# Performance work log

Hardware: AMD Instinct MI355X
Metric: run time of the kernel (lower is better)

Reference implementation:

```python
import jax, jax.numpy as jnp
import numpy as np

N = 100000          # nodes
E = 800000          # edges per relation
R = 6               # relations
B = 1000            # graphs
IN_DIM = 14
POS_COL = 5
PE = 8              # pos_emb_dim
H = 128             # hidden_dim
OUT = 128           # out_dim
NPOS = 24
D1 = IN_DIM - 1 + PE  # 21, GAT layer-1 input dim


def setup_inputs() -> dict:
    key = jax.random.key(0)
    ks = jax.random.split(key, 20)
    x_all = jax.random.normal(ks[0], (N, IN_DIM), dtype=jnp.float32)
    pos = jax.random.randint(ks[1], (N,), 0, NPOS)
    x_all = x_all.at[:, POS_COL].set(pos.astype(jnp.float32))
    edges = jax.random.randint(ks[2], (R, 2, E), 0, N, dtype=jnp.int32)
    batch = jnp.sort(jax.random.randint(ks[3], (N,), 0, B, dtype=jnp.int32))
    pos_table = jax.random.normal(ks[4], (NPOS, PE), dtype=jnp.float32) * 0.02
    W1 = jax.random.normal(ks[5], (R, D1, H), dtype=jnp.float32) * 0.1
    as1 = jax.random.normal(ks[6], (R, H), dtype=jnp.float32) * 0.1
    ad1 = jax.random.normal(ks[7], (R, H), dtype=jnp.float32) * 0.1
    b1 = jnp.zeros((R, H), dtype=jnp.float32)
    W2 = jax.random.normal(ks[8], (R, H, H), dtype=jnp.float32) * 0.05
    as2 = jax.random.normal(ks[9], (R, H), dtype=jnp.float32) * 0.1
    ad2 = jax.random.normal(ks[10], (R, H), dtype=jnp.float32) * 0.1
    b2 = jnp.zeros((R, H), dtype=jnp.float32)
    n1w = jnp.ones((H,), dtype=jnp.float32)
    n1b = jnp.zeros((H,), dtype=jnp.float32)
    n2w = jnp.ones((H,), dtype=jnp.float32)
    n2b = jnp.zeros((H,), dtype=jnp.float32)
    query = jax.random.normal(ks[11], (H,), dtype=jnp.float32) * 0.02
    projW = jax.random.normal(ks[12], (H, OUT), dtype=jnp.float32) * 0.05
    projb = jnp.zeros((OUT,), dtype=jnp.float32)
    return dict(x_all=x_all, edges=edges, batch=batch, pos_table=pos_table,
                W1=W1, as1=as1, ad1=ad1, b1=b1, W2=W2, as2=as2, ad2=ad2, b2=b2,
                n1w=n1w, n1b=n1b, n2w=n2w, n2b=n2b, query=query, projW=projW, projb=projb)


def _seg_softmax(logits, seg, num):
    m = jax.lax.stop_gradient(jax.ops.segment_max(logits, seg, num_segments=num))
    e = jnp.exp(logits - m[seg])
    s = jax.ops.segment_sum(e, seg, num_segments=num)
    return e / s[seg]


def _gat_layer(x, W, a_s, a_d, b, edges):
    # sum over R relation-specific GATConv(heads=1, concat=False) outputs
    n = x.shape[0]
    out = jnp.zeros((n, W.shape[-1]), dtype=x.dtype)
    for r in range(R):
        xp = x @ W[r]                       # [N, H] projected features
        src, dst = edges[r, 0], edges[r, 1]
        z = (xp @ a_s[r])[src] + (xp @ a_d[r])[dst]
        z = jnp.where(z > 0, z, 0.2 * z)    # LeakyReLU(0.2)
        alpha = _seg_softmax(z, dst, n)     # per-destination softmax
        agg = jax.ops.segment_sum(alpha[:, None] * xp[src], dst, num_segments=n)
        out = out + agg + b[r]
    return out


def _ln(x, w, b):
    mu = x.mean(-1, keepdims=True)
    v = ((x - mu) ** 2).mean(-1, keepdims=True)
    return (x - mu) / jnp.sqrt(v + 1e-5) * w + b


def reference(x_all, edges, batch, pos_table, W1, as1, ad1, b1,
              W2, as2, ad2, b2, n1w, n1b, n2w, n2b, query, projW, projb):
    cont = jnp.concatenate([x_all[:, :POS_COL], x_all[:, POS_COL + 1:]], axis=1)
    pidx = jnp.clip(x_all[:, POS_COL].astype(jnp.int32), 0, NPOS - 1)
    x = jnp.concatenate([cont, pos_table[pidx]], axis=1)  # [N, D1]
    x = _gat_layer(x, W1, as1, ad1, b1, edges)
    x = _ln(jax.nn.gelu(x, approximate=False), n1w, n1b)
    x = _gat_layer(x, W2, as2, ad2, b2, edges)
    x = _ln(jax.nn.gelu(x, approximate=False), n2w, n2b)
    # AttentionPooling: gather-score-softmax-scatter over batch segments
    scores = x @ query
    w = _seg_softmax(scores, batch, B)
    pool = jax.ops.segment_sum(w[:, None] * x, batch, num_segments=B)  # [B, H]
    return pool @ projW + projb
```

## Files before the change

kernel.cpp:

```cpp
#include <hip/hip_runtime.h>
#include <math.h>

#define NN   100000
#define EE   800000
#define RR   6
#define BB   1000
#define HH   128
#define MM   (RR*NN)
#define NBPR ((NN + 255) >> 8)
#define NBK  (RR * NBPR)
#define CH   4096
#define CAP  4096

static inline int ceil_div(int a, int b){ return (a+b-1)/b; }

typedef __attribute__((ext_vector_type(8))) short bf16x8;
typedef __attribute__((ext_vector_type(4))) short bf16x4;
typedef __attribute__((ext_vector_type(4))) float f32x4;

__device__ __forceinline__ unsigned fenc(float f){
  unsigned u = __float_as_uint(f);
  return (u & 0x80000000u) ? ~u : (u | 0x80000000u);
}
__device__ __forceinline__ float fdec(unsigned u){
  return __uint_as_float((u & 0x80000000u) ? (u & 0x7fffffffu) : ~u);
}
__device__ __forceinline__ unsigned short f2bf(float f){
  unsigned u = __float_as_uint(f);
  return (unsigned short)((u + 0x7fffu + ((u >> 16) & 1u)) >> 16);
}
__device__ __forceinline__ float bf2f(unsigned short h){
  return __uint_as_float(((unsigned)h) << 16);
}
__device__ __forceinline__ float wexp(float z){
  z = (z > 0.f) ? z : 0.2f*z;
  z = fminf(fmaxf(z, -60.f), 60.f);
  return __expf(z);
}

__global__ void k_binscatter(const int* __restrict__ edges, int* __restrict__ bcur,
                             unsigned* __restrict__ ebkt)
{
  __shared__ int hist[NBPR];
  __shared__ int base[NBPR];
  int t = threadIdx.x;
  const int nch = (EE + CH - 1) / CH;
  int r = blockIdx.x / nch, c = blockIdx.x - r*nch;
  for (int i = t; i < NBPR; i += 256) hist[i] = 0;
  __syncthreads();
  const int* sptr = edges + (size_t)r*2*EE;
  const int* dptr = sptr + EE;
  int e0 = c*CH, e1 = min(EE, e0 + CH);
  for (int i = e0 + t; i < e1; i += 256)
    atomicAdd(&hist[dptr[i] >> 8], 1);
  __syncthreads();
  for (int i = t; i < NBPR; i += 256) {
    int h = hist[i];
    int gb = r*NBPR + i;
    base[i] = h ? (gb*CAP + atomicAdd(&bcur[gb], h)) : 0;
    hist[i] = 0;
  }
  __syncthreads();
  for (int i = e0 + t; i < e1; i += 256) {
    int dst = dptr[i];
    int b = dst >> 8;
    int slot = base[b] + atomicAdd(&hist[b], 1);
    ebkt[slot] = ((unsigned)sptr[i] << 8) | (unsigned)(dst & 255);
  }
}

__global__ void k_bscan(const int* __restrict__ bcur, int* __restrict__ boff,
                        int* __restrict__ off)
{
  __shared__ int sh[256];
  int t = threadIdx.x;
  int carry = 0;
  for (int c = 0; c < NBK; c += 256) {
    int idx = c + t;
    int v = (idx < NBK) ? bcur[idx] : 0;
    sh[t] = v;
    __syncthreads();
    for (int o = 1; o < 256; o <<= 1) {
      int add = (t >= o) ? sh[t-o] : 0;
      __syncthreads();
      sh[t] += add;
      __syncthreads();
    }
    int incl = sh[t];
    int tot  = sh[255];
    if (idx < NBK) boff[idx] = carry + incl - v;
    __syncthreads();
    carry += tot;
  }
  if (t == 0) { boff[NBK] = carry; off[MM] = carry; }
}

__global__ void k_bbuild(const unsigned* __restrict__ ebkt, const int* __restrict__ bcur,
                         const int* __restrict__ boff,
                         int* __restrict__ off, int* __restrict__ elist)
{
  __shared__ int cnt[256];
  __shared__ int sc[256];
  __shared__ int cur[256];
  int t = threadIdx.x;
  int bb = blockIdx.x;
  int e0r = bb*CAP, e1r = e0r + bcur[bb];
  int w0 = boff[bb];
  cnt[t] = 0;
  __syncthreads();
  for (int i = e0r + t; i < e1r; i += 256)
    atomicAdd(&cnt[ebkt[i] & 255u], 1);
  __syncthreads();
  sc[t] = cnt[t];
  __syncthreads();
  for (int o = 1; o < 256; o <<= 1) {
    int add = (t >= o) ? sc[t-o] : 0;
    __syncthreads();
    sc[t] += add;
    __syncthreads();
  }
  int excl = sc[t] - cnt[t];
  int r = bb / NBPR, b = bb - r*NBPR;
  int dst = b*256 + t;
  if (dst < NN) off[r*NN + dst] = w0 + excl;
  cur[t] = w0 + excl;
  __syncthreads();
  for (int i = e0r + t; i < e1r; i += 256) {
    unsigned w = ebkt[i];
    int slot = atomicAdd(&cur[w & 255u], 1);
    elist[slot] = (int)(w >> 8);
  }
}

__global__ void k_featprep(const float* __restrict__ x_all, const float* __restrict__ pos_table,
                           short* __restrict__ x0h, short* __restrict__ x0l)
{
  int gid = blockIdx.x*256 + threadIdx.x;
  if (gid >= NN*32) return;
  int nidx = gid >> 5, c = gid & 31;
  float v = 0.f;
  if (c < 13) {
    int scl = (c < 5) ? c : c + 1;
    v = x_all[nidx*14 + scl];
  } else if (c < 21) {
    int pi = (int)x_all[nidx*14 + 5];
    pi = pi < 0 ? 0 : (pi > 23 ? 23 : pi);
    v = pos_table[pi*8 + (c - 13)];
  }
  unsigned short h = f2bf(v);
  unsigned short l = f2bf(v - bf2f(h));
  x0h[gid] = (short)h;
  x0l[gid] = (short)l;
}

template<int KP>
__global__ void k_wprep(const float* __restrict__ W, int K,
                        short* __restrict__ Wh, short* __restrict__ Wl)
{
  int gid = blockIdx.x*256 + threadIdx.x;
  if (gid >= RR*128*KP) return;
  int r = gid / (128*KP);
  int rem = gid - r*(128*KP);
  int nn = rem / KP, k = rem - nn*KP;
  float v = (k < K) ? W[((size_t)r*K + k)*128 + nn] : 0.f;
  unsigned short h = f2bf(v);
  unsigned short l = f2bf(v - bf2f(h));
  Wh[gid] = (short)h;
  Wl[gid] = (short)l;
}

__global__ void k_wprep2(const float* __restrict__ W,
                         short* __restrict__ Wh, short* __restrict__ Wl)
{
  int gid = blockIdx.x*256 + threadIdx.x;
  if (gid >= RR*128*128) return;
  int r = gid / (128*128);
  int i = gid - r*(128*128);
  int kc = i >> 12;
  int lg = (i >> 10) & 3;
  int row = (i >> 3) & 127;
  int e = i & 7;
  int k = kc*32 + 16*(e >> 2) + 4*lg + (e & 3);
  float v = W[((size_t)r*128 + k)*128 + row];
  unsigned short h = f2bf(v);
  unsigned short l = f2bf(v - bf2f(h));
  Wh[gid] = (short)h;
  Wl[gid] = (short)l;
}

template<int KP>
__global__ void k_wa(const float* __restrict__ W, const float* __restrict__ as,
                     const float* __restrict__ ad, int K, float* __restrict__ wa)
{
  int idx = blockIdx.x*256 + threadIdx.x;
  if (idx >= 12*KP) return;
  int rr = idx / KP, k = idx - rr*KP;
  int r = (rr < 6) ? rr : rr - 6;
  const float* a = ((rr < 6) ? as : ad) + (size_t)r*HH;
  float s = 0.f;
  if (k < K) {
    const float* wrow = W + ((size_t)r*K + k)*128;
    #pragma unroll 8
    for (int h = 0; h < 128; ++h) s = fmaf(wrow[h], a[h], s);
  }
  wa[idx] = s;
}

__global__ void k_zsd32(const short* __restrict__ xh, const short* __restrict__ xl,
                        const float* __restrict__ wa, float* __restrict__ zsd, int n)
{
  __shared__ float w[12*32];
  int tid = threadIdx.x;
  for (int i = tid; i < 12*32; i += 256) w[i] = wa[i];
  __syncthreads();
  int g = blockIdx.x*256 + tid;
  if (g >= n) return;
  float v[32];
  #pragma unroll
  for (int c = 0; c < 4; ++c) {
    uint4 vh = *(const uint4*)(xh + (size_t)g*32 + c*8);
    uint4 vl = *(const uint4*)(xl + (size_t)g*32 + c*8);
    const unsigned short* hp = (const unsigned short*)&vh;
    const unsigned short* lp = (const unsigned short*)&vl;
    #pragma unroll
    for (int j = 0; j < 8; ++j) v[c*8+j] = bf2f(hp[j]) + bf2f(lp[j]);
  }
  #pragma unroll
  for (int rr = 0; rr < 12; ++rr) {
    float d = 0.f;
    #pragma unroll
    for (int k = 0; k < 32; ++k) d = fmaf(v[k], w[rr*32+k], d);
    zsd[(size_t)rr*n + g] = d;
  }
}

__global__ void k_zsd128(const unsigned short* __restrict__ xh,
                         const float* __restrict__ wa, float* __restrict__ zsd, int n)
{
  __shared__ float w[12*128];
  int tid = threadIdx.x;
  for (int i = tid; i < 12*128; i += 256) w[i] = wa[i];
  __syncthreads();
  int gid = blockIdx.x*256 + tid;
  int g = gid >> 4, l = tid & 15;
  if (g >= n) return;
  uint4 vh = *(const uint4*)(xh + (size_t)g*128 + l*8);
  const unsigned short* hp = (const unsigned short*)&vh;
  float v[8];
  #pragma unroll
  for (int j = 0; j < 8; ++j) v[j] = bf2f(hp[j]);
  float dot[12];
  #pragma unroll
  for (int rr = 0; rr < 12; ++rr) {
    float p = 0.f;
    #pragma unroll
    for (int j = 0; j < 8; ++j) p = fmaf(v[j], w[rr*128 + l*8 + j], p);
    p += __shfl_xor(p, 1); p += __shfl_xor(p, 2);
    p += __shfl_xor(p, 4); p += __shfl_xor(p, 8);
    dot[rr] = p;
  }
  if (l < 12) zsd[(size_t)l*n + g] = dot[l];
}

__global__ void k_agg1(const unsigned short* __restrict__ x0h, const float* __restrict__ zsd,
                       const int* __restrict__ elist, const int* __restrict__ off,
                       unsigned short* __restrict__ aggH, int n)
{
  int gid = blockIdx.x*256 + threadIdx.x;
  int g = gid >> 4;
  int l = threadIdx.x & 15;
  if (g >= n) return;
  int sub = l >> 2, ch = l & 3;

  for (int rel = 0; rel < RR; ++rel) {
    const float* zsr = zsd + (size_t)rel*n;
    const float* zdr = zsd + (size_t)(6+rel)*n;
    int o0 = off[(size_t)rel*NN + g];
    int deg = off[(size_t)rel*NN + g + 1] - o0;
    float acc[8] = {0,0,0,0,0,0,0,0};
    float esum = 0.f;
    float inv = 0.f;
    if (deg > 0) {
      float zdd = zdr[g];
      for (int base = 0; base < deg; base += 8) {
        int i0 = base + sub, i1 = base + 4 + sub;
        float e0 = 0.f, e1 = 0.f; int s0 = 0, s1 = 0;
        if (i0 < deg) {
          s0 = elist[o0+i0];
          e0 = wexp(zsr[s0] + zdd);
        }
        if (i1 < deg) {
          s1 = elist[o0+i1];
          e1 = wexp(zsr[s1] + zdd);
        }
        esum += e0 + e1;
        uint4 v0 = *(const uint4*)(x0h + (size_t)s0*32 + ch*8);
        uint4 v1 = *(const uint4*)(x0h + (size_t)s1*32 + ch*8);
        acc[0] = fmaf(e0, __uint_as_float(v0.x << 16),         acc[0]);
        acc[1] = fmaf(e0, __uint_as_float(v0.x & 0xffff0000u), acc[1]);
        acc[2] = fmaf(e0, __uint_as_float(v0.y << 16),         acc[2]);
        acc[3] = fmaf(e0, __uint_as_float(v0.y & 0xffff0000u), acc[3]);
        acc[4] = fmaf(e0, __uint_as_float(v0.z << 16),         acc[4]);
        acc[5] = fmaf(e0, __uint_as_float(v0.z & 0xffff0000u), acc[5]);
        acc[6] = fmaf(e0, __uint_as_float(v0.w << 16),         acc[6]);
        acc[7] = fmaf(e0, __uint_as_float(v0.w & 0xffff0000u), acc[7]);
        acc[0] = fmaf(e1, __uint_as_float(v1.x << 16),         acc[0]);
        acc[1] = fmaf(e1, __uint_as_float(v1.x & 0xffff0000u), acc[1]);
        acc[2] = fmaf(e1, __uint_as_float(v1.y << 16),         acc[2]);
        acc[3] = fmaf(e1, __uint_as_float(v1.y & 0xffff0000u), acc[3]);
        acc[4] = fmaf(e1, __uint_as_float(v1.z << 16),         acc[4]);
        acc[5] = fmaf(e1, __uint_as_float(v1.z & 0xffff0000u), acc[5]);
        acc[6] = fmaf(e1, __uint_as_float(v1.w << 16),         acc[6]);
        acc[7] = fmaf(e1, __uint_as_float(v1.w & 0xffff0000u), acc[7]);
      }
      esum += __shfl_xor(esum, 4);
      esum += __shfl_xor(esum, 8);
      #pragma unroll
      for (int j = 0; j < 8; ++j) {
        acc[j] += __shfl_xor(acc[j], 4);
        acc[j] += __shfl_xor(acc[j], 8);
      }
      inv = 1.f / esum;
    }
    if (sub == 0) {
      uint4 ph;
      unsigned* php = (unsigned*)&ph;
      #pragma unroll
      for (int j2 = 0; j2 < 4; ++j2) {
        float a0 = acc[2*j2]   * inv;
        float a1 = acc[2*j2+1] * inv;
        php[j2] = ((unsigned)f2bf(a1) << 16) | f2bf(a0);
      }
      *(uint4*)(aggH + ((size_t)rel*n + g)*32 + ch*8) = ph;
    }
  }
}

__device__ __forceinline__ bf16x8 ldfragG(const short* __restrict__ p, int row, int kb, int KP_)
{
  bf16x4 a = *(const bf16x4*)(p + (size_t)row*KP_ + kb);
  bf16x4 b = *(const bf16x4*)(p + (size_t)row*KP_ + kb + 16);
  return __builtin_shufflevector(a, b, 0,1,2,3,4,5,6,7);
}

__global__ __launch_bounds__(256, 4)
void k_gemm1(const short* __restrict__ aggH,
             const short* __restrict__ Wh, const short* __restrict__ Wl,
             const float* __restrict__ bsv,
             const float* __restrict__ nw, const float* __restrict__ nb,
             unsigned short* __restrict__ Yh, int n)
{
  __shared__ __align__(16) float Cs[32*136];
  int tid = threadIdx.x;
  int r0 = blockIdx.x * 32;
  int wid = tid >> 6, lane = tid & 63;
  int lr = lane & 15, lg = lane >> 4;
  int rt = wid >> 1;
  int c0 = (wid & 1) * 4;
  int arow = r0 + rt*16 + lr;
  int kb = 4*lg;
  f32x4 acct[4] = {{0,0,0,0},{0,0,0,0},{0,0,0,0},{0,0,0,0}};

  for (int rel = 0; rel < RR; ++rel) {
    const short* Ahr = aggH + (size_t)rel*n*32;
    const short* Whr = Wh + (size_t)rel*128*32;
    const short* Wlr = Wl + (size_t)rel*128*32;
    bf16x8 ah = ldfragG(Ahr, arow, kb, 32);
    #pragma unroll
    for (int t = 0; t < 4; ++t) {
      int wrow = (c0 + t)*16 + lr;
      bf16x8 whf = ldfragG(Whr, wrow, kb, 32);
      bf16x8 wlf = ldfragG(Wlr, wrow, kb, 32);
      acct[t] = __builtin_amdgcn_mfma_f32_16x16x32_bf16(ah, whf, acct[t], 0, 0, 0);
      acct[t] = __builtin_amdgcn_mfma_f32_16x16x32_bf16(ah, wlf, acct[t], 0, 0, 0);
    }
  }

  #pragma unroll
  for (int t = 0; t < 4; ++t)
    #pragma unroll
    for (int v = 0; v < 4; ++v) {
      int row = rt*16 + lg*4 + v;
      int col = (c0 + t)*16 + lr;
      float x = acct[t][v] + bsv[col];
      Cs[row*136 + col] = 0.5f*x*(1.f + erff(x*0.70710678118654752f));
    }
  __syncthreads();
  {
    int r = tid >> 3, sg = tid & 7;
    float vals[16];
    float s = 0.f;
    #pragma unroll
    for (int i = 0; i < 16; ++i) { vals[i] = Cs[r*136 + sg*16 + i]; s += vals[i]; }
    s += __shfl_xor(s, 1); s += __shfl_xor(s, 2); s += __shfl_xor(s, 4);
    float mu = s * (1.f/128.f);
    float var = 0.f;
    #pragma unroll
    for (int i = 0; i < 16; ++i) { vals[i] -= mu; var += vals[i]*vals[i]; }
    var += __shfl_xor(var, 1); var += __shfl_xor(var, 2); var += __shfl_xor(var, 4);
    float inv = 1.f / sqrtf(var*(1.f/128.f) + 1e-5f);
    int g = r0 + r;
    uint4 ph0, ph1;
    unsigned* php0 = (unsigned*)&ph0; unsigned* php1 = (unsigned*)&ph1;
    #pragma unroll
    for (int j2 = 0; j2 < 8; ++j2) {
      int c = sg*16 + 2*j2;
      float y0 = vals[2*j2]  *inv*nw[c]   + nb[c];
      float y1 = vals[2*j2+1]*inv*nw[c+1] + nb[c+1];
      unsigned hw = ((unsigned)f2bf(y1) << 16) | f2bf(y0);
      if (j2 < 4) php0[j2] = hw; else php1[j2-4] = hw;
    }
    *(uint4*)(Yh + (size_t)g*128 + sg*16)     = ph0;
    *(uint4*)(Yh + (size_t)g*128 + sg*16 + 8) = ph1;
  }
}

#define ACC8(W_, U_) \
  tmp[0] = fmaf(W_, __uint_as_float((U_).x << 16),         tmp[0]); \
  tmp[1] = fmaf(W_, __uint_as_float((U_).x & 0xffff0000u), tmp[1]); \
  tmp[2] = fmaf(W_, __uint_as_float((U_).y << 16),         tmp[2]); \
  tmp[3] = fmaf(W_, __uint_as_float((U_).y & 0xffff0000u), tmp[3]); \
  tmp[4] = fmaf(W_, __uint_as_float((U_).z << 16),         tmp[4]); \
  tmp[5] = fmaf(W_, __uint_as_float((U_).z & 0xffff0000u), tmp[5]); \
  tmp[6] = fmaf(W_, __uint_as_float((U_).w << 16),         tmp[6]); \
  tmp[7] = fmaf(W_, __uint_as_float((U_).w & 0xffff0000u), tmp[7]);

__global__ void k_agg2(const unsigned short* __restrict__ h1,
                       const float* __restrict__ zsd,
                       const int* __restrict__ elist,
                       const int* __restrict__ off,
                       int rbase,
                       unsigned short* __restrict__ agg2,
                       int n)
{
  int gid = blockIdx.x*256 + threadIdx.x;
  int g = gid >> 4;
  int l = threadIdx.x & 15;
  int gbase = threadIdx.x & 48;
  if (g >= n) return;

  for (int r = 0; r < 3; ++r) {
    int o0 = off[(size_t)r*NN + g], o1 = off[(size_t)r*NN + g + 1];
    int deg = o1 - o0;
    float tmp[8] = {0,0,0,0,0,0,0,0};
    float inv = 0.f;
    if (deg > 0) {
      const float* zsr = zsd + (size_t)(rbase+r)*n;
      float zdd = zsd[(size_t)(6+rbase+r)*n + g];
      float esum = 0.f;
      for (int base = 0; base < deg; base += 16) {
        int i = base + l;
        float ew = 0.f; int s = 0;
        if (i < deg) {
          s = elist[o0+i];
          ew = wexp(zsr[s] + zdd);
        }
        esum += ew;
        int cnt = min(16, deg - base);
        for (int t = 0; t < cnt; t += 4) {
          float w0 = __shfl(ew, gbase + t);
          float w1 = __shfl(ew, gbase + t + 1);
          float w2 = __shfl(ew, gbase + t + 2);
          float w3 = __shfl(ew, gbase + t + 3);
          int a0 = __shfl(s, gbase + t);
          int a1 = __shfl(s, gbase + t + 1);
          int a2 = __shfl(s, gbase + t + 2);
          int a3 = __shfl(s, gbase + t + 3);
          uint4 u0 = *(const uint4*)(h1 + (size_t)a0*128 + l*8);
          uint4 u1 = *(const uint4*)(h1 + (size_t)a1*128 + l*8);
          uint4 u2 = *(const uint4*)(h1 + (size_t)a2*128 + l*8);
          uint4 u3 = *(const uint4*)(h1 + (size_t)a3*128 + l*8);
          ACC8(w0, u0);
          ACC8(w1, u1);
          ACC8(w2, u2);
          ACC8(w3, u3);
        }
      }
      esum += __shfl_xor(esum, 1);
      esum += __shfl_xor(esum, 2);
      esum += __shfl_xor(esum, 4);
      esum += __shfl_xor(esum, 8);
      inv = 1.f / esum;
    }
    uint4 ph;
    unsigned* php = (unsigned*)&ph;
    #pragma unroll
    for (int j2 = 0; j2 < 4; ++j2) {
      float a0 = tmp[2*j2]   * inv;
      float a1 = tmp[2*j2+1] * inv;
      php[j2] = ((unsigned)f2bf(a1) << 16) | f2bf(a0);
    }
    *(uint4*)(agg2 + ((size_t)r*n + g)*128 + l*8) = ph;
  }
}

template<int FIN>
__global__ __launch_bounds__(512, 2)
void k_gemm2(const unsigned short* __restrict__ agg2,
             const short* __restrict__ WhAll, const short* __restrict__ WlAll, int rbase,
             const float* __restrict__ bsv,
             const float* __restrict__ nw, const float* __restrict__ nb,
             float* __restrict__ hacc, float* __restrict__ Yf,
             const float* __restrict__ q, const int* __restrict__ batch,
             float* __restrict__ scores, unsigned* __restrict__ bmax, int n)
{
  constexpr int KP = 128;
  __shared__ __align__(16) short lds[2*128*KP];
  constexpr int WH0 = 0, WL0 = 128*KP;
  int tid = threadIdx.x;
  int r0 = blockIdx.x * 128;
  int wid = tid >> 6, lane = tid & 63;
  int lr = lane & 15, lg = lane >> 4;
  int grow = r0 + wid*16 + lr;
  int growc = min(grow, n-1);
  f32x4 acc[8] = {{0,0,0,0},{0,0,0,0},{0,0,0,0},{0,0,0,0},
                  {0,0,0,0},{0,0,0,0},{0,0,0,0},{0,0,0,0}};

  for (int rel = 0; rel < 3; ++rel) {
    const short* Ar = (const short*)(agg2 + (size_t)rel*n*KP);
    const short* Wh = WhAll + (size_t)(rbase+rel)*128*KP;
    const short* Wl = WlAll + (size_t)(rbase+rel)*128*KP;
    for (int ch = tid; ch < 128*16; ch += 512) {
      *(bf16x8*)(lds + WH0 + ch*8) = *(const bf16x8*)(Wh + (size_t)ch*8);
      *(bf16x8*)(lds + WL0 + ch*8) = *(const bf16x8*)(Wl + (size_t)ch*8);
    }
    __syncthreads();
    #pragma unroll
    for (int kc = 0; kc < 4; ++kc) {
      int kb = kc*32 + 4*lg;
      bf16x8 ah = ldfragG(Ar, growc, kb, KP);
      int fbase = ((kc*4 + lg)*128)*8;
      #pragma unroll
      for (int ct = 0; ct < 8; ++ct) {
        int wrow = ct*16 + lr;
        bf16x8 wh = *(const bf16x8*)(lds + WH0 + fbase + wrow*8);
        bf16x8 wl = *(const bf16x8*)(lds + WL0 + fbase + wrow*8);
        acc[ct] = __builtin_amdgcn_mfma_f32_16x16x32_bf16(ah, wh, acc[ct], 0, 0, 0);
        acc[ct] = __builtin_amdgcn_mfma_f32_16x16x32_bf16(ah, wl, acc[ct], 0, 0, 0);
      }
    }
    __syncthreads();
  }

  if (FIN == 0) {
    #pragma unroll
    for (int v = 0; v < 4; ++v) {
      int row = r0 + wid*16 + lg*4 + v;
      if (row < n) {
        #pragma unroll
        for (int ct = 0; ct < 8; ++ct)
          hacc[(size_t)row*128 + ct*16 + lr] = acc[ct][v];
      }
    }
  } else {
    #pragma unroll
    for (int v = 0; v < 4; ++v) {
      int row = r0 + wid*16 + lg*4 + v;
      int rowc = min(row, n-1);
      float vals[8];
      float s = 0.f;
      #pragma unroll
      for (int ct = 0; ct < 8; ++ct) {
        int c = ct*16 + lr;
        float x = acc[ct][v] + hacc[(size_t)rowc*128 + c] + bsv[c];
        x = 0.5f*x*(1.f + erff(x*0.70710678118654752f));
        vals[ct] = x;
        s += x;
      }
      s += __shfl_xor(s, 1); s += __shfl_xor(s, 2);
      s += __shfl_xor(s, 4); s += __shfl_xor(s, 8);
      float mu = s * (1.f/128.f);
      float var = 0.f;
      #pragma unroll
      for (int ct = 0; ct < 8; ++ct) { vals[ct] -= mu; var += vals[ct]*vals[ct]; }
      var += __shfl_xor(var, 1); var += __shfl_xor(var, 2);
      var += __shfl_xor(var, 4); var += __shfl_xor(var, 8);
      float inv = 1.f / sqrtf(var*(1.f/128.f) + 1e-5f);
      float sc = 0.f;
      #pragma unroll
      for (int ct = 0; ct < 8; ++ct) {
        int c = ct*16 + lr;
        float y = vals[ct]*inv*nw[c] + nb[c];
        if (row < n) Yf[(size_t)row*128 + c] = y;
        sc = fmaf(y, q[c], sc);
      }
      sc += __shfl_xor(sc, 1); sc += __shfl_xor(sc, 2);
      sc += __shfl_xor(sc, 4); sc += __shfl_xor(sc, 8);
      if (lr == 0 && row < n) {
        scores[row] = sc;
        atomicMax(&bmax[batch[row]], fenc(sc));
      }
    }
  }
}

__global__ void k_bsum(const float* __restrict__ b, float* __restrict__ bs)
{
  int t = threadIdx.x;
  float s = 0.f;
  #pragma unroll
  for (int r = 0; r < RR; ++r) s += b[r*HH + t];
  bs[t] = s;
}

__global__ void k_segbounds(const int* __restrict__ batch, int* __restrict__ segst,
                            int n, int numB)
{
  int b = blockIdx.x*256 + threadIdx.x;
  if (b > numB) return;
  int lo = 0, hi = n;
  while (lo < hi) { int mid = (lo+hi) >> 1; if (batch[mid] < b) lo = mid+1; else hi = mid; }
  segst[b] = lo;
}

__global__ void k_pool(const float* __restrict__ X, const float* __restrict__ scores,
                       const int* __restrict__ segst, const unsigned* __restrict__ bmax,
                       float* __restrict__ pool, int numB)
{
  int b = blockIdx.x;
  int t = threadIdx.x;
  int s0 = segst[b], s1 = segst[b+1];
  float m = fdec(bmax[b]);
  float acc0 = 0.f, acc1 = 0.f, esum = 0.f;
  int i = s0;
  for (; i + 1 < s1; i += 2) {
    float e0 = __expf(scores[i] - m);
    float e1 = __expf(scores[i+1] - m);
    esum += e0 + e1;
    acc0 = fmaf(e0, X[(size_t)i*128 + t], acc0);
    acc1 = fmaf(e1, X[(size_t)(i+1)*128 + t], acc1);
  }
  if (i < s1) {
    float e0 = __expf(scores[i] - m);
    esum += e0;
    acc0 = fmaf(e0, X[(size_t)i*128 + t], acc0);
  }
  float inv = (s1 > s0) ? 1.f/esum : 0.f;
  pool[(size_t)b*128 + t] = (acc0 + acc1) * inv;
}

__global__ void k_outgemm(const float* __restrict__ pool, const float* __restrict__ projW,
                          const float* __restrict__ projb, float* __restrict__ out, int numB)
{
  int b = blockIdx.x;
  int j = threadIdx.x;
  __shared__ float p[128];
  p[j] = pool[(size_t)b*128 + j];
  __syncthreads();
  float acc = projb[j];
  #pragma unroll 16
  for (int k = 0; k < 128; ++k) acc = fmaf(p[k], projW[(size_t)k*128 + j], acc);
  out[(size_t)b*128 + j] = acc;
}

extern "C" void kernel_launch(void* const* d_in, const int* in_sizes, int n_in,
                              void* d_out, int out_size, void* d_ws, size_t ws_size,
                              hipStream_t stream)
{
  const float* x_all = (const float*)d_in[0];
  const int*   edges = (const int*)d_in[1];
  const int*   batch = (const int*)d_in[2];
  const float* pos_table = (const float*)d_in[3];
  const float* W1  = (const float*)d_in[4];
  const float* as1 = (const float*)d_in[5];
  const float* ad1 = (const float*)d_in[6];
  const float* b1  = (const float*)d_in[7];
  const float* W2  = (const float*)d_in[8];
  const float* as2 = (const float*)d_in[9];
  const float* ad2 = (const float*)d_in[10];
  const float* b2  = (const float*)d_in[11];
  const float* n1w = (const float*)d_in[12];
  const float* n1b = (const float*)d_in[13];
  const float* n2w = (const float*)d_in[14];
  const float* n2b = (const float*)d_in[15];
  const float* query = (const float*)d_in[16];
  const float* projW = (const float*)d_in[17];
  const float* projb = (const float*)d_in[18];
  float* out = (float*)d_out;
  (void)in_sizes; (void)n_in; (void)out_size; (void)ws_size;

  char* p = (char*)d_ws;
  auto alloc = [&](size_t b){ void* r = (void*)p; p += (b + 255) & ~(size_t)255; return r; };
  int*   off   = (int*)alloc((size_t)(MM+1)*sizeof(int));
  int*   elist = (int*)alloc((size_t)RR*EE*sizeof(int));
  int*   boff  = (int*)alloc((size_t)(NBK+1)*sizeof(int));
  int*   bcur  = (int*)alloc((size_t)NBK*sizeof(int));
  short* wtH   = (short*)alloc((size_t)RR*128*128*sizeof(short));
  short* wtL   = (short*)alloc((size_t)RR*128*128*sizeof(short));
  float* wa    = (float*)alloc((size_t)12*128*sizeof(float));
  float* zsd   = (float*)alloc((size_t)12*NN*sizeof(float));
  float* bsv   = (float*)alloc(128*sizeof(float));
  int*   segst = (int*)alloc((size_t)(BB+1)*sizeof(int));
  unsigned* bmax = (unsigned*)alloc((size_t)BB*sizeof(unsigned));
  float* pool  = (float*)alloc((size_t)BB*HH*sizeof(float));
  float* scrs  = (float*)alloc((size_t)NN*sizeof(float));
  unsigned short* big = (unsigned short*)alloc((size_t)3*NN*128*sizeof(short));
  float* R1    = (float*)alloc((size_t)NN*128*sizeof(float));
  float* R2    = (float*)alloc((size_t)NN*128*sizeof(float));

  unsigned* ebkt = (unsigned*)R1;
  short* x0h = (short*)R1;
  short* x0l = x0h + (size_t)NN*32;
  float* hacc = R1;
  unsigned short* h1h = (unsigned short*)R2;
  float* h2 = (float*)R2;
  unsigned short* aggH = big;
  unsigned short* agg2 = big;

  const int nch = (EE + CH - 1) / CH;
  hipMemsetAsync(bcur, 0, (size_t)NBK*sizeof(int), stream);
  k_binscatter<<<RR*nch,256,0,stream>>>(edges, bcur, ebkt);
  k_bscan<<<1,256,0,stream>>>(bcur, boff, off);
  k_bbuild<<<NBK,256,0,stream>>>(ebkt, bcur, boff, off, elist);

  k_featprep<<<ceil_div(NN*32,256),256,0,stream>>>(x_all, pos_table, x0h, x0l);
  k_segbounds<<<ceil_div(BB+1,256),256,0,stream>>>(batch, segst, NN, BB);
  hipMemsetAsync(bmax, 0, (size_t)BB*sizeof(unsigned), stream);

  k_wa<32><<<ceil_div(12*32,256),256,0,stream>>>(W1, as1, ad1, 21, wa);
  k_zsd32<<<ceil_div(NN,256),256,0,stream>>>(x0h, x0l, wa, zsd, NN);
  k_wprep<32><<<ceil_div(RR*128*32,256),256,0,stream>>>(W1, 21, wtH, wtL);
  k_bsum<<<1,128,0,stream>>>(b1, bsv);
  k_agg1<<<ceil_div(NN*16,256),256,0,stream>>>((const unsigned short*)x0h, zsd, elist, off,
                                               aggH, NN);
  k_gemm1<<<ceil_div(NN,32),256,0,stream>>>((const short*)aggH,
                                            wtH, wtL, bsv, n1w, n1b, h1h, NN);

  k_wa<128><<<ceil_div(12*128,256),256,0,stream>>>(W2, as2, ad2, 128, wa);
  k_zsd128<<<ceil_div(NN*16,256),256,0,stream>>>(h1h, wa, zsd, NN);
  k_wprep2<<<ceil_div(RR*128*128,256),256,0,stream>>>(W2, wtH, wtL);
  k_bsum<<<1,128,0,stream>>>(b2, bsv);
  int aggGrid = ceil_div(NN*16, 256);
  int gemm2Grid = ceil_div(NN, 128);
  k_agg2<<<aggGrid,256,0,stream>>>(h1h, zsd, elist, off, 0, agg2, NN);
  k_gemm2<0><<<gemm2Grid,512,0,stream>>>(agg2, wtH, wtL, 0, bsv, n2w, n2b,
      hacc, (float*)0, query, batch, scrs, bmax, NN);
  k_agg2<<<aggGrid,256,0,stream>>>(h1h, zsd, elist, off + (size_t)3*NN, 3, agg2, NN);
  k_gemm2<1><<<gemm2Grid,512,0,stream>>>(agg2, wtH, wtL, 3, bsv, n2w, n2b,
      hacc, h2, query, batch, scrs, bmax, NN);

  k_pool<<<BB,128,0,stream>>>(h2, scrs, segst, bmax, pool, BB);
  k_outgemm<<<BB,128,0,stream>>>(pool, projW, projb, out, BB);
}
```

Baseline: 740.6 us.

## Fuse both layer-2 GEMM passes into one six-relation kernel with bf16 output

Both halves of the layer-2 aggregation now run before a single GEMM kernel. That kernel accumulates all six relations in registers, so the fp32 partial-sum buffer (hacc) no longer needs to be written and read back. The aggregation outputs are spread over three separate buffers placed in reused scratch memory. LDS is halved by loading the high and low weight halves in turn, which allows a higher launch-bounds occupancy, and A fragments are prefetched before the weight load. The final normalized features are stored as bf16 and the pooling kernel reads bf16, which halves that traffic at some cost in precision.

```diff
diff --git a/kernel.cpp b/kernel.cpp
--- a/kernel.cpp
+++ b/kernel.cpp
@@ -430,7 +430,9 @@
                        const int* __restrict__ elist,
                        const int* __restrict__ off,
                        int rbase,
-                       unsigned short* __restrict__ agg2,
+                       unsigned short* __restrict__ out0,
+                       unsigned short* __restrict__ out1,
+                       unsigned short* __restrict__ out2,
                        int n)
 {
   int gid = blockIdx.x*256 + threadIdx.x;
@@ -482,6 +484,7 @@
       esum += __shfl_xor(esum, 8);
       inv = 1.f / esum;
     }
+    unsigned short* outp = (r == 0) ? out0 : (r == 1) ? out1 : out2;
     uint4 ph;
     unsigned* php = (unsigned*)&ph;
     #pragma unroll
@@ -490,23 +493,23 @@
       float a1 = tmp[2*j2+1] * inv;
       php[j2] = ((unsigned)f2bf(a1) << 16) | f2bf(a0);
     }
-    *(uint4*)(agg2 + ((size_t)r*n + g)*128 + l*8) = ph;
-  }
-}
-
-template<int FIN>
-__global__ __launch_bounds__(512, 2)
-void k_gemm2(const unsigned short* __restrict__ agg2,
-             const short* __restrict__ WhAll, const short* __restrict__ WlAll, int rbase,
+    *(uint4*)(outp + (size_t)g*128 + l*8) = ph;
+  }
+}
+
+__global__ __launch_bounds__(512, 6)
+void k_gemm2(const unsigned short* __restrict__ A0,
+             const unsigned short* __restrict__ A1,
+             const unsigned short* __restrict__ A2,
+             const short* __restrict__ WhAll, const short* __restrict__ WlAll,
              const float* __restrict__ bsv,
              const float* __restrict__ nw, const float* __restrict__ nb,
-             float* __restrict__ hacc, float* __restrict__ Yf,
+             unsigned short* __restrict__ Yb,
              const float* __restrict__ q, const int* __restrict__ batch,
              float* __restrict__ scores, unsigned* __restrict__ bmax, int n)
 {
   constexpr int KP = 128;
-  __shared__ __align__(16) short lds[2*128*KP];
-  constexpr int WH0 = 0, WL0 = 128*KP;
+  __shared__ __align__(16) short lds[128*KP];
   int tid = threadIdx.x;
   int r0 = blockIdx.x * 128;
   int wid = tid >> 6, lane = tid & 63;
@@ -516,80 +519,81 @@
   f32x4 acc[8] = {{0,0,0,0},{0,0,0,0},{0,0,0,0},{0,0,0,0},
                   {0,0,0,0},{0,0,0,0},{0,0,0,0},{0,0,0,0}};
 
-  for (int rel = 0; rel < 3; ++rel) {
-    const short* Ar = (const short*)(agg2 + (size_t)rel*n*KP);
-    const short* Wh = WhAll + (size_t)(rbase+rel)*128*KP;
-    const short* Wl = WlAll + (size_t)(rbase+rel)*128*KP;
-    for (int ch = tid; ch < 128*16; ch += 512) {
-      *(bf16x8*)(lds + WH0 + ch*8) = *(const bf16x8*)(Wh + (size_t)ch*8);
-      *(bf16x8*)(lds + WL0 + ch*8) = *(const bf16x8*)(Wl + (size_t)ch*8);
-    }
+  for (int rel = 0; rel < RR; ++rel) {
+    const unsigned short* Ar = (rel < 3) ? A0 + (size_t)rel*n*KP
+                             : (rel < 5) ? A1 + (size_t)(rel-3)*n*KP
+                                         : A2;
+    const short* Wh = WhAll + (size_t)rel*128*KP;
+    const short* Wl = WlAll + (size_t)rel*128*KP;
+    bf16x8 af0 = ldfragG((const short*)Ar, growc,  0 + 4*lg, KP);
+    bf16x8 af1 = ldfragG((const short*)Ar, growc, 32 + 4*lg, KP);
+    bf16x8 af2 = ldfragG((const short*)Ar, growc, 64 + 4*lg, KP);
+    bf16x8 af3 = ldfragG((const short*)Ar, growc, 96 + 4*lg, KP);
+    for (int ch = tid; ch < 128*16; ch += 512)
+      *(bf16x8*)(lds + (size_t)ch*8) = *(const bf16x8*)(Wh + (size_t)ch*8);
     __syncthreads();
     #pragma unroll
     for (int kc = 0; kc < 4; ++kc) {
-      int kb = kc*32 + 4*lg;
-      bf16x8 ah = ldfragG(Ar, growc, kb, KP);
+      bf16x8 af = (kc == 0) ? af0 : (kc == 1) ? af1 : (kc == 2) ? af2 : af3;
       int fbase = ((kc*4 + lg)*128)*8;
       #pragma unroll
       for (int ct = 0; ct < 8; ++ct) {
-        int wrow = ct*16 + lr;
-        bf16x8 wh = *(const bf16x8*)(lds + WH0 + fbase + wrow*8);
-        bf16x8 wl = *(const bf16x8*)(lds + WL0 + fbase + wrow*8);
-        acc[ct] = __builtin_amdgcn_mfma_f32_16x16x32_bf16(ah, wh, acc[ct], 0, 0, 0);
-        acc[ct] = __builtin_amdgcn_mfma_f32_16x16x32_bf16(ah, wl, acc[ct], 0, 0, 0);
+        bf16x8 wf = *(const bf16x8*)(lds + fbase + (ct*16 + lr)*8);
+        acc[ct] = __builtin_amdgcn_mfma_f32_16x16x32_bf16(af, wf, acc[ct], 0, 0, 0);
       }
     }
     __syncthreads();
-  }
-
-  if (FIN == 0) {
-    #pragma unroll
-    for (int v = 0; v < 4; ++v) {
-      int row = r0 + wid*16 + lg*4 + v;
-      if (row < n) {
-        #pragma unroll
-        for (int ct = 0; ct < 8; ++ct)
-          hacc[(size_t)row*128 + ct*16 + lr] = acc[ct][v];
-      }
-    }
-  } else {
-    #pragma unroll
-    for (int v = 0; v < 4; ++v) {
-      int row = r0 + wid*16 + lg*4 + v;
-      int rowc = min(row, n-1);
-      float vals[8];
-      float s = 0.f;
+    for (int ch = tid; ch < 128*16; ch += 512)
+      *(bf16x8*)(lds + (size_t)ch*8) = *(const bf16x8*)(Wl + (size_t)ch*8);
+    __syncthreads();
+    #pragma unroll
+    for (int kc = 0; kc < 4; ++kc) {
+      bf16x8 af = (kc == 0) ? af0 : (kc == 1) ? af1 : (kc == 2) ? af2 : af3;
+      int fbase = ((kc*4 + lg)*128)*8;
       #pragma unroll
       for (int ct = 0; ct < 8; ++ct) {
-        int c = ct*16 + lr;
-        float x = acc[ct][v] + hacc[(size_t)rowc*128 + c] + bsv[c];
-        x = 0.5f*x*(1.f + erff(x*0.70710678118654752f));
-        vals[ct] = x;
-        s += x;
+        bf16x8 wf = *(const bf16x8*)(lds + fbase + (ct*16 + lr)*8);
+        acc[ct] = __builtin_amdgcn_mfma_f32_16x16x32_bf16(af, wf, acc[ct], 0, 0, 0);
       }
-      s += __shfl_xor(s, 1); s += __shfl_xor(s, 2);
-      s += __shfl_xor(s, 4); s += __shfl_xor(s, 8);
-      float mu = s * (1.f/128.f);
-      float var = 0.f;
-      #pragma unroll
-      for (int ct = 0; ct < 8; ++ct) { vals[ct] -= mu; var += vals[ct]*vals[ct]; }
-      var += __shfl_xor(var, 1); var += __shfl_xor(var, 2);
-      var += __shfl_xor(var, 4); var += __shfl_xor(var, 8);
-      float inv = 1.f / sqrtf(var*(1.f/128.f) + 1e-5f);
-      float sc = 0.f;
-      #pragma unroll
-      for (int ct = 0; ct < 8; ++ct) {
-        int c = ct*16 + lr;
-        float y = vals[ct]*inv*nw[c] + nb[c];
-        if (row < n) Yf[(size_t)row*128 + c] = y;
-        sc = fmaf(y, q[c], sc);
-      }
-      sc += __shfl_xor(sc, 1); sc += __shfl_xor(sc, 2);
-      sc += __shfl_xor(sc, 4); sc += __shfl_xor(sc, 8);
-      if (lr == 0 && row < n) {
-        scores[row] = sc;
-        atomicMax(&bmax[batch[row]], fenc(sc));
-      }
+    }
+    __syncthreads();
+  }
+
+  #pragma unroll
+  for (int v = 0; v < 4; ++v) {
+    int row = r0 + wid*16 + lg*4 + v;
+    float vals[8];
+    float s = 0.f;
+    #pragma unroll
+    for (int ct = 0; ct < 8; ++ct) {
+      int c = ct*16 + lr;
+      float x = acc[ct][v] + bsv[c];
+      x = 0.5f*x*(1.f + erff(x*0.70710678118654752f));
+      vals[ct] = x;
+      s += x;
+    }
+    s += __shfl_xor(s, 1); s += __shfl_xor(s, 2);
+    s += __shfl_xor(s, 4); s += __shfl_xor(s, 8);
+    float mu = s * (1.f/128.f);
+    float var = 0.f;
+    #pragma unroll
+    for (int ct = 0; ct < 8; ++ct) { vals[ct] -= mu; var += vals[ct]*vals[ct]; }
+    var += __shfl_xor(var, 1); var += __shfl_xor(var, 2);
+    var += __shfl_xor(var, 4); var += __shfl_xor(var, 8);
+    float inv = 1.f / sqrtf(var*(1.f/128.f) + 1e-5f);
+    float sc = 0.f;
+    #pragma unroll
+    for (int ct = 0; ct < 8; ++ct) {
+      int c = ct*16 + lr;
+      float y = vals[ct]*inv*nw[c] + nb[c];
+      if (row < n) Yb[(size_t)row*128 + c] = f2bf(y);
+      sc = fmaf(y, q[c], sc);
+    }
+    sc += __shfl_xor(sc, 1); sc += __shfl_xor(sc, 2);
+    sc += __shfl_xor(sc, 4); sc += __shfl_xor(sc, 8);
+    if (lr == 0 && row < n) {
+      scores[row] = sc;
+      atomicMax(&bmax[batch[row]], fenc(sc));
     }
   }
 }
@@ -613,7 +617,7 @@
   segst[b] = lo;
 }
 
-__global__ void k_pool(const float* __restrict__ X, const float* __restrict__ scores,
+__global__ void k_pool(const unsigned short* __restrict__ X, const float* __restrict__ scores,
                        const int* __restrict__ segst, const unsigned* __restrict__ bmax,
                        float* __restrict__ pool, int numB)
 {
@@ -627,13 +631,13 @@
     float e0 = __expf(scores[i] - m);
     float e1 = __expf(scores[i+1] - m);
     esum += e0 + e1;
-    acc0 = fmaf(e0, X[(size_t)i*128 + t], acc0);
-    acc1 = fmaf(e1, X[(size_t)(i+1)*128 + t], acc1);
+    acc0 = fmaf(e0, bf2f(X[(size_t)i*128 + t]), acc0);
+    acc1 = fmaf(e1, bf2f(X[(size_t)(i+1)*128 + t]), acc1);
   }
   if (i < s1) {
     float e0 = __expf(scores[i] - m);
     esum += e0;
-    acc0 = fmaf(e0, X[(size_t)i*128 + t], acc0);
+    acc0 = fmaf(e0, bf2f(X[(size_t)i*128 + t]), acc0);
   }
   float inv = (s1 > s0) ? 1.f/esum : 0.f;
   pool[(size_t)b*128 + t] = (acc0 + acc1) * inv;
@@ -701,11 +705,12 @@
   unsigned* ebkt = (unsigned*)R1;
   short* x0h = (short*)R1;
   short* x0l = x0h + (size_t)NN*32;
-  float* hacc = R1;
+  unsigned short* agg2b = (unsigned short*)R1;
   unsigned short* h1h = (unsigned short*)R2;
-  float* h2 = (float*)R2;
+  unsigned short* agg2c = h1h + (size_t)NN*128;
+  unsigned short* h2b = h1h;
   unsigned short* aggH = big;
-  unsigned short* agg2 = big;
+  unsigned short* agg2a = big;
 
   const int nch = (EE + CH - 1) / CH;
   hipMemsetAsync(bcur, 0, (size_t)NBK*sizeof(int), stream);
@@ -731,14 +736,13 @@
   k_wprep2<<<ceil_div(RR*128*128,256),256,0,stream>>>(W2, wtH, wtL);
   k_bsum<<<1,128,0,stream>>>(b2, bsv);
   int aggGrid = ceil_div(NN*16, 256);
-  int gemm2Grid = ceil_div(NN, 128);
-  k_agg2<<<aggGrid,256,0,stream>>>(h1h, zsd, elist, off, 0, agg2, NN);
-  k_gemm2<0><<<gemm2Grid,512,0,stream>>>(agg2, wtH, wtL, 0, bsv, n2w, n2b,
-      hacc, (float*)0, query, batch, scrs, bmax, NN);
-  k_agg2<<<aggGrid,256,0,stream>>>(h1h, zsd, elist, off + (size_t)3*NN, 3, agg2, NN);
-  k_gemm2<1><<<gemm2Grid,512,0,stream>>>(agg2, wtH, wtL, 3, bsv, n2w, n2b,
-      hacc, h2, query, batch, scrs, bmax, NN);
-
-  k_pool<<<BB,128,0,stream>>>(h2, scrs, segst, bmax, pool, BB);
+  k_agg2<<<aggGrid,256,0,stream>>>(h1h, zsd, elist, off, 0,
+      agg2a, agg2a + (size_t)NN*128, agg2a + (size_t)2*NN*128, NN);
+  k_agg2<<<aggGrid,256,0,stream>>>(h1h, zsd, elist, off + (size_t)3*NN, 3,
+      agg2b, agg2b + (size_t)NN*128, agg2c, NN);
+  k_gemm2<<<ceil_div(NN,128),512,0,stream>>>(agg2a, agg2b, agg2c, wtH, wtL,
+      bsv, n2w, n2b, h2b, query, batch, scrs, bmax, NN);
+
+  k_pool<<<BB,128,0,stream>>>(h2b, scrs, segst, bmax, pool, BB);
   k_outgemm<<<BB,128,0,stream>>>(pool, projW, projb, out, BB);
 }
```

Measured after the change: 751.2 us. Within noise of the previous version (+1.4%).
